# Kernel optimization log

Measured on AMD Instinct MI355X. Metric: run time of the kernel, lower is better.

## Reference

```python
import jax, jax.numpy as jnp
import numpy as np

N = 50000      # num nodes
E = 800000     # edges per hypergraph (avg degree 16)
G = 3          # hyper_edge_num
D_IN = 128
D_OUT = 128


def setup_inputs() -> dict:
    key = jax.random.key(0)
    ks = jax.random.split(key, 6)
    company_emb = jax.random.normal(ks[0], (N, D_IN), dtype=jnp.float32)
    # nn.Linear weight [out, in], glorot-ish scaling
    W = jax.random.normal(ks[1], (D_OUT, D_IN), dtype=jnp.float32) / np.sqrt(D_IN).astype(np.float32)
    alpha = jax.random.normal(ks[2], (G, 1), dtype=jnp.float32)
    edge_rows = jax.random.randint(ks[3], (G, E), 0, N, dtype=jnp.int32)
    edge_cols = jax.random.randint(ks[4], (G, E), 0, N, dtype=jnp.int32)
    edge_vals = jax.random.normal(ks[5], (G, E), dtype=jnp.float32)
    return {
        "company_emb": company_emb,
        "W": W,
        "alpha": alpha,
        "edge_rows": edge_rows,
        "edge_cols": edge_cols,
        "edge_vals": edge_vals,
    }


def reference(company_emb, W, alpha, edge_rows, edge_cols, edge_vals):
    # shared dense projection: h = X @ W^T, [N, D_OUT]
    h = company_emb @ W.T

    def spmm(rows, cols, vals):
        # sparse Laplacian (COO) @ h : gather source rows, scale, scatter-add to dest rows
        msg = vals[:, None] * h[cols]                     # [E, D_OUT]
        return jax.ops.segment_sum(msg, rows, num_segments=N)

    aggs = jax.vmap(spmm)(edge_rows, edge_cols, edge_vals)  # [G, N, D_OUT]
    gate = jax.nn.sigmoid(alpha[:, 0])                       # [G]
    # res = sum_g sigmoid(alpha_g) * (L_g @ h)
    return jnp.einsum('g,gnd->nd', gate, aggs)
```

## Files before the change

kernel.cpp:

```cpp
#include <hip/hip_runtime.h>
#include <math.h>

#define NNODES 50000
#define NEDGE  800000
#define NG     3
#define D      128
#define GE     (NG*NEDGE)
#define NBUK   782
#define CH     4096
#define NBLK   ((GE + CH - 1) / CH)
#define OS     (NBUK + 1)
#define CAP2   3456

typedef __attribute__((ext_vector_type(8))) short bf16x8;
typedef __attribute__((ext_vector_type(4))) float f32x4;

__device__ __forceinline__ unsigned short f2bf(float f) {
    unsigned u = __float_as_uint(f);
    return (unsigned short)((u + 0x7fffu + ((u >> 16) & 1u)) >> 16);
}

__global__ void k_wprep(const float* __restrict__ W, uint4* __restrict__ Wf) {
    const int t = threadIdx.x;
    for (int i = t; i < 2048; i += 256) {
        const int nt   = i >> 8;
        const int kc   = (i >> 6) & 3;
        const int lane = i & 63;
        const int n  = nt * 16 + (lane & 15);
        const int k0 = kc * 32 + (lane >> 4) * 8;
        const float* src = W + (size_t)n * 128 + k0;
        unsigned u0 = (unsigned)f2bf(src[0]) | ((unsigned)f2bf(src[1]) << 16);
        unsigned u1 = (unsigned)f2bf(src[2]) | ((unsigned)f2bf(src[3]) << 16);
        unsigned u2 = (unsigned)f2bf(src[4]) | ((unsigned)f2bf(src[5]) << 16);
        unsigned u3 = (unsigned)f2bf(src[6]) | ((unsigned)f2bf(src[7]) << 16);
        Wf[i] = make_uint4(u0, u1, u2, u3);
    }
}

__global__ __launch_bounds__(256) void k_gemm(const float* __restrict__ X,
                                              const uint4* __restrict__ Wf,
                                              unsigned short* __restrict__ hb16) {
    __shared__ uint4 Wl[2048];
    const int t = threadIdx.x;
#pragma unroll
    for (int j = 0; j < 8; ++j) Wl[t + j * 256] = Wf[t + j * 256];
    __syncthreads();

    const int w    = t >> 6;
    const int lane = t & 63;
    const int q    = lane >> 4;
    const int ml   = lane & 15;
    const int m0   = blockIdx.x * 64 + w * 16;

    int xr = m0 + ml; if (xr >= NNODES) xr = NNODES - 1;
    const float* xrow = X + (size_t)xr * 128;

    bf16x8 xf[4];
#pragma unroll
    for (int kc = 0; kc < 4; ++kc) {
        const int k0 = kc * 32 + q * 8;
        float4 a = *(const float4*)(xrow + k0);
        float4 b = *(const float4*)(xrow + k0 + 4);
        bf16x8 v;
        v[0] = (short)f2bf(a.x); v[1] = (short)f2bf(a.y);
        v[2] = (short)f2bf(a.z); v[3] = (short)f2bf(a.w);
        v[4] = (short)f2bf(b.x); v[5] = (short)f2bf(b.y);
        v[6] = (short)f2bf(b.z); v[7] = (short)f2bf(b.w);
        xf[kc] = v;
    }

#pragma unroll
    for (int nt = 0; nt < 8; ++nt) {
        f32x4 acc = {0.f, 0.f, 0.f, 0.f};
#pragma unroll
        for (int kc = 0; kc < 4; ++kc) {
            const bf16x8 wf = *(const bf16x8*)&Wl[(nt * 4 + kc) * 64 + lane];
            acc = __builtin_amdgcn_mfma_f32_16x16x32_bf16(xf[kc], wf, acc, 0, 0, 0);
        }
#pragma unroll
        for (int r = 0; r < 4; ++r) {
            const int row = m0 + q * 4 + r;
            if (row < NNODES)
                hb16[(size_t)row * 128 + nt * 16 + ml] = f2bf(acc[r]);
        }
    }
}

__global__ __launch_bounds__(256) void k_bin(const int* __restrict__ rows,
                                             const int* __restrict__ cols,
                                             const float* __restrict__ vals,
                                             const float* __restrict__ alpha,
                                             uint2* __restrict__ out1,
                                             int* __restrict__ off1) {
    __shared__ uint2 stg[CH];
    __shared__ unsigned short rnk[CH];
    __shared__ int sA[1024];
    const int t   = threadIdx.x;
    const int blk = blockIdx.x;
    const int start = blk * CH;
    const int end   = (start + CH < GE) ? (start + CH) : GE;

    const float g0 = 1.0f / (1.0f + __expf(-alpha[0]));
    const float g1 = 1.0f / (1.0f + __expf(-alpha[1]));
    const float g2 = 1.0f / (1.0f + __expf(-alpha[2]));

#pragma unroll
    for (int j = 0; j < 4; ++j) sA[t + j * 256] = 0;
    __syncthreads();

    for (int idx = start + t, k = t; idx < end; idx += 256, k += 256) {
        const int r = rows[idx];
        const int c = cols[idx];
        const float v = vals[idx];
        const float gv = v * (idx < NEDGE ? g0 : (idx < 2 * NEDGE ? g1 : g2));
        uint2 rec;
        rec.x = ((unsigned)r << 16) | (unsigned)c;
        rec.y = __float_as_uint(gv);
        stg[k] = rec;
        rnk[k] = (unsigned short)atomicAdd(&sA[r >> 6], 1);
    }
    __syncthreads();

    for (int off = 1; off < 1024; off <<= 1) {
        int v[4];
#pragma unroll
        for (int j = 0; j < 4; ++j) {
            const int i = t + j * 256;
            v[j] = sA[i] + ((i >= off) ? sA[i - off] : 0);
        }
        __syncthreads();
#pragma unroll
        for (int j = 0; j < 4; ++j) sA[t + j * 256] = v[j];
        __syncthreads();
    }

    for (int b = t; b < NBUK; b += 256)
        off1[(size_t)blk * OS + b] = b ? sA[b - 1] : 0;
    if (t == 0) off1[(size_t)blk * OS + NBUK] = sA[NBUK - 1];

    for (int idx = start + t, k = t; idx < end; idx += 256, k += 256) {
        const uint2 rec = stg[k];
        const int b = (int)(rec.x >> 22);
        const int pos = (b ? sA[b - 1] : 0) + (int)rnk[k];
        out1[(size_t)blk * CH + pos] = rec;
    }
}

__global__ __launch_bounds__(512) void k_agg2(const unsigned* __restrict__ hbits,
                                              const uint2* __restrict__ out1,
                                              const int* __restrict__ off1,
                                              float* __restrict__ out) {
    __shared__ uint2 stg[CAP2];
    __shared__ unsigned short order[CAP2];
    __shared__ int sA[512];
    __shared__ int sB[512];
    __shared__ int rh[64], rbase[64], rcur[64];
    const int t = threadIdx.x;
    const int b = blockIdx.x;

    if (t < 64) rh[t] = 0;

    const int s0 = off1[(size_t)t * OS + b];
    const int e0 = off1[(size_t)t * OS + b + 1];
    int s1 = 0, e1 = 0;
    int myLen = e0 - s0;
    if (t + 512 < NBLK) {
        s1 = off1[(size_t)(t + 512) * OS + b];
        e1 = off1[(size_t)(t + 512) * OS + b + 1];
        myLen += e1 - s1;
    }
    sA[t] = myLen;
    __syncthreads();

    int* src = sA; int* dst = sB;
    for (int off = 1; off < 512; off <<= 1) {
        dst[t] = src[t] + ((t >= off) ? src[t - off] : 0);
        __syncthreads();
        int* tmp = src; src = dst; dst = tmp;
    }
    const int base = src[t] - myLen;

    {
        int p = base;
        const uint2* seg = out1 + (size_t)t * CH;
        for (int i = s0; i < e0; ++i, ++p) {
            if (p < CAP2) {
                const uint2 rec = seg[i];
                stg[p] = rec;
                atomicAdd(&rh[(rec.x >> 16) & 63u], 1);
            }
        }
        if (t + 512 < NBLK) {
            const uint2* seg2 = out1 + (size_t)(t + 512) * CH;
            for (int i = s1; i < e1; ++i, ++p) {
                if (p < CAP2) {
                    const uint2 rec = seg2[i];
                    stg[p] = rec;
                    atomicAdd(&rh[(rec.x >> 16) & 63u], 1);
                }
            }
        }
    }
    __syncthreads();

    if (t < 64) sA[t] = rh[t];
    __syncthreads();
    for (int off = 1; off < 64; off <<= 1) {
        int v = 0;
        if (t < 64) v = sA[t] + ((t >= off) ? sA[t - off] : 0);
        __syncthreads();
        if (t < 64) sA[t] = v;
        __syncthreads();
    }
    if (t < 64) { rbase[t] = sA[t] - rh[t]; rcur[t] = sA[t] - rh[t]; }
    __syncthreads();

    {
        const int lim = (base + myLen < CAP2) ? (base + myLen) : CAP2;
        for (int k = base; k < lim; ++k) {
            const int lr = (int)((stg[k].x >> 16) & 63u);
            const int pos = atomicAdd(&rcur[lr], 1);
            order[pos] = (unsigned short)k;
        }
    }
    __syncthreads();

    const int w    = t >> 6;
    const int lane = t & 63;
    for (int k = 0; k < 8; ++k) {
        const int lr  = (w << 3) + k;
        const int row = (b << 6) + lr;
        const int s   = rbase[lr];
        const int cnt = rh[lr];
        float2 acc = make_float2(0.f, 0.f);
        int i = 0;
        for (; i + 8 <= cnt; i += 8) {
            int idx8[8];
#pragma unroll
            for (int j = 0; j < 8; ++j) idx8[j] = order[s + i + j];
            uint2 m[8];
#pragma unroll
            for (int j = 0; j < 8; ++j) m[j] = stg[idx8[j]];
            unsigned hb[8];
#pragma unroll
            for (int j = 0; j < 8; ++j)
                hb[j] = hbits[(size_t)(m[j].x & 0xffffu) * 64 + lane];
#pragma unroll
            for (int j = 0; j < 8; ++j) {
                const float v = __uint_as_float(m[j].y);
                acc.x += v * __uint_as_float(hb[j] << 16);
                acc.y += v * __uint_as_float(hb[j] & 0xffff0000u);
            }
        }
        for (; i < cnt; ++i) {
            const uint2 m = stg[order[s + i]];
            const unsigned hbv = hbits[(size_t)(m.x & 0xffffu) * 64 + lane];
            const float v = __uint_as_float(m.y);
            acc.x += v * __uint_as_float(hbv << 16);
            acc.y += v * __uint_as_float(hbv & 0xffff0000u);
        }
        if (row < NNODES)
            ((float2*)out)[(size_t)row * 64 + lane] = acc;
    }
}

extern "C" void kernel_launch(void* const* d_in, const int* in_sizes, int n_in,
                              void* d_out, int out_size, void* d_ws, size_t ws_size,
                              hipStream_t stream) {
    const float* X     = (const float*)d_in[0];
    const float* W     = (const float*)d_in[1];
    const float* alpha = (const float*)d_in[2];
    const int*   rows  = (const int*)d_in[3];
    const int*   cols  = (const int*)d_in[4];
    const float* vals  = (const float*)d_in[5];
    float* out = (float*)d_out;

    char* ws = (char*)d_ws;
    unsigned*       hbits = (unsigned*)(ws + 0);
    unsigned short* hb16  = (unsigned short*)(ws + 0);
    uint2*          out1  = (uint2*)(ws + 12800000);
    int*            off1  = (int*)  (ws + 32002048);
    uint4*          Wf    = (uint4*)(ws + 33837408);

    hipLaunchKernelGGL(k_wprep, dim3(1), dim3(256), 0, stream, W, Wf);
    hipLaunchKernelGGL(k_gemm, dim3(NBUK), dim3(256), 0, stream, X, Wf, hb16);
    hipLaunchKernelGGL(k_bin, dim3(NBLK), dim3(256), 0, stream,
                       rows, cols, vals, alpha, out1, off1);
    hipLaunchKernelGGL(k_agg2, dim3(NBUK), dim3(512), 0, stream,
                       hbits, out1, off1, out);
}
```

Before: 240.1 us.

## Rebucket rows into 768 variable-width buckets and sort edges directly into SoA shared layout

Destination rows are binned into 768 buckets of about 65 rows each (computed as r*48/3125), so the aggregation grid matches a multiple of the CU count. The aggregation kernel drops the per-thread prefix scan and indirect order array. It counts rows in a first pass, then scatters column indices and values straight into padded structure-of-arrays shared buffers. This allows vectorised 16-byte LDS reads of eight edges at a time, at the cost of reading each segment from global memory twice and clamping buckets that exceed the 4096-entry capacity.

```diff
diff --git a/kernel.cpp b/kernel.cpp
--- a/kernel.cpp
+++ b/kernel.cpp
@@ -6,11 +6,12 @@
 #define NG     3
 #define D      128
 #define GE     (NG*NEDGE)
-#define NBUK   782
+#define NBUK   768
+#define GEMMB  782
 #define CH     4096
 #define NBLK   ((GE + CH - 1) / CH)
 #define OS     (NBUK + 1)
-#define CAP2   3456
+#define CAP    4096
 
 typedef __attribute__((ext_vector_type(8))) short bf16x8;
 typedef __attribute__((ext_vector_type(4))) float f32x4;
@@ -18,6 +19,10 @@
 __device__ __forceinline__ unsigned short f2bf(float f) {
     unsigned u = __float_as_uint(f);
     return (unsigned short)((u + 0x7fffu + ((u >> 16) & 1u)) >> 16);
+}
+
+__device__ __forceinline__ int bucket_of(unsigned r) {
+    return (int)((r * 48u) / 3125u);
 }
 
 __global__ void k_wprep(const float* __restrict__ W, uint4* __restrict__ Wf) {
@@ -117,7 +122,7 @@
         rec.x = ((unsigned)r << 16) | (unsigned)c;
         rec.y = __float_as_uint(gv);
         stg[k] = rec;
-        rnk[k] = (unsigned short)atomicAdd(&sA[r >> 6], 1);
+        rnk[k] = (unsigned short)atomicAdd(&sA[bucket_of((unsigned)r)], 1);
     }
     __syncthreads();
 
@@ -140,127 +145,125 @@
 
     for (int idx = start + t, k = t; idx < end; idx += 256, k += 256) {
         const uint2 rec = stg[k];
-        const int b = (int)(rec.x >> 22);
+        const int b = bucket_of(rec.x >> 16);
         const int pos = (b ? sA[b - 1] : 0) + (int)rnk[k];
         out1[(size_t)blk * CH + pos] = rec;
     }
 }
 
-__global__ __launch_bounds__(512) void k_agg2(const unsigned* __restrict__ hbits,
+__global__ __launch_bounds__(512) void k_agg3(const unsigned* __restrict__ hbits,
                                               const uint2* __restrict__ out1,
                                               const int* __restrict__ off1,
                                               float* __restrict__ out) {
-    __shared__ uint2 stg[CAP2];
-    __shared__ unsigned short order[CAP2];
-    __shared__ int sA[512];
-    __shared__ int sB[512];
-    __shared__ int rh[64], rbase[64], rcur[64];
+    __shared__ __align__(16) unsigned short colS[CAP];
+    __shared__ __align__(16) float          valS[CAP];
+    __shared__ int rh[72], rbase[72], rcur[72];
+    __shared__ int sS[128];
     const int t = threadIdx.x;
     const int b = blockIdx.x;
 
-    if (t < 64) rh[t] = 0;
+    const int sstart = (b * 3125 + 47) / 48;
+    const int send   = ((b + 1) * 3125 + 47) / 48;
+    const int width  = send - sstart;
+
+    if (t < 72) rh[t] = 0;
 
     const int s0 = off1[(size_t)t * OS + b];
     const int e0 = off1[(size_t)t * OS + b + 1];
     int s1 = 0, e1 = 0;
-    int myLen = e0 - s0;
     if (t + 512 < NBLK) {
         s1 = off1[(size_t)(t + 512) * OS + b];
         e1 = off1[(size_t)(t + 512) * OS + b + 1];
-        myLen += e1 - s1;
-    }
-    sA[t] = myLen;
-    __syncthreads();
-
-    int* src = sA; int* dst = sB;
-    for (int off = 1; off < 512; off <<= 1) {
-        dst[t] = src[t] + ((t >= off) ? src[t - off] : 0);
-        __syncthreads();
-        int* tmp = src; src = dst; dst = tmp;
-    }
-    const int base = src[t] - myLen;
+    }
+    __syncthreads();
 
     {
-        int p = base;
         const uint2* seg = out1 + (size_t)t * CH;
-        for (int i = s0; i < e0; ++i, ++p) {
-            if (p < CAP2) {
-                const uint2 rec = seg[i];
-                stg[p] = rec;
-                atomicAdd(&rh[(rec.x >> 16) & 63u], 1);
+        for (int i = s0; i < e0; ++i)
+            atomicAdd(&rh[(int)(seg[i].x >> 16) - sstart], 1);
+        const uint2* seg2 = out1 + (size_t)(t + 512) * CH;
+        for (int i = s1; i < e1; ++i)
+            atomicAdd(&rh[(int)(seg2[i].x >> 16) - sstart], 1);
+    }
+    __syncthreads();
+
+    if (t < 128) sS[t] = (t < width) ? ((rh[t] + 7) & ~7) : 0;
+    __syncthreads();
+    for (int off = 1; off < 128; off <<= 1) {
+        int v = 0;
+        if (t < 128) v = sS[t] + ((t >= off) ? sS[t - off] : 0);
+        __syncthreads();
+        if (t < 128) sS[t] = v;
+        __syncthreads();
+    }
+    if (t < width) {
+        const int rb = sS[t] - ((rh[t] + 7) & ~7);
+        rbase[t] = rb;
+        rcur[t]  = rb;
+    }
+    __syncthreads();
+
+    {
+        const uint2* seg = out1 + (size_t)t * CH;
+        for (int i = s0; i < e0; ++i) {
+            const uint2 rec = seg[i];
+            const int lr  = (int)(rec.x >> 16) - sstart;
+            const int pos = atomicAdd(&rcur[lr], 1);
+            if (pos < CAP) {
+                colS[pos] = (unsigned short)(rec.x & 0xffffu);
+                valS[pos] = __uint_as_float(rec.y);
             }
         }
-        if (t + 512 < NBLK) {
-            const uint2* seg2 = out1 + (size_t)(t + 512) * CH;
-            for (int i = s1; i < e1; ++i, ++p) {
-                if (p < CAP2) {
-                    const uint2 rec = seg2[i];
-                    stg[p] = rec;
-                    atomicAdd(&rh[(rec.x >> 16) & 63u], 1);
-                }
+        const uint2* seg2 = out1 + (size_t)(t + 512) * CH;
+        for (int i = s1; i < e1; ++i) {
+            const uint2 rec = seg2[i];
+            const int lr  = (int)(rec.x >> 16) - sstart;
+            const int pos = atomicAdd(&rcur[lr], 1);
+            if (pos < CAP) {
+                colS[pos] = (unsigned short)(rec.x & 0xffffu);
+                valS[pos] = __uint_as_float(rec.y);
             }
-        }
-    }
-    __syncthreads();
-
-    if (t < 64) sA[t] = rh[t];
-    __syncthreads();
-    for (int off = 1; off < 64; off <<= 1) {
-        int v = 0;
-        if (t < 64) v = sA[t] + ((t >= off) ? sA[t - off] : 0);
-        __syncthreads();
-        if (t < 64) sA[t] = v;
-        __syncthreads();
-    }
-    if (t < 64) { rbase[t] = sA[t] - rh[t]; rcur[t] = sA[t] - rh[t]; }
-    __syncthreads();
-
-    {
-        const int lim = (base + myLen < CAP2) ? (base + myLen) : CAP2;
-        for (int k = base; k < lim; ++k) {
-            const int lr = (int)((stg[k].x >> 16) & 63u);
-            const int pos = atomicAdd(&rcur[lr], 1);
-            order[pos] = (unsigned short)k;
         }
     }
     __syncthreads();
 
     const int w    = t >> 6;
     const int lane = t & 63;
-    for (int k = 0; k < 8; ++k) {
-        const int lr  = (w << 3) + k;
-        const int row = (b << 6) + lr;
-        const int s   = rbase[lr];
-        const int cnt = rh[lr];
+    for (int lr = w; lr < width; lr += 8) {
+        const int s = rbase[lr];
+        int cnt = rh[lr];
+        if (s + cnt > CAP) cnt = (CAP > s) ? (CAP - s) : 0;
         float2 acc = make_float2(0.f, 0.f);
         int i = 0;
         for (; i + 8 <= cnt; i += 8) {
-            int idx8[8];
-#pragma unroll
-            for (int j = 0; j < 8; ++j) idx8[j] = order[s + i + j];
-            uint2 m[8];
-#pragma unroll
-            for (int j = 0; j < 8; ++j) m[j] = stg[idx8[j]];
+            const uint4  cv = *(const uint4*)&colS[s + i];
+            const float4 va = *(const float4*)&valS[s + i];
+            const float4 vb = *(const float4*)&valS[s + i + 4];
             unsigned hb[8];
-#pragma unroll
-            for (int j = 0; j < 8; ++j)
-                hb[j] = hbits[(size_t)(m[j].x & 0xffffu) * 64 + lane];
+            hb[0] = hbits[(size_t)(cv.x & 0xffffu) * 64 + lane];
+            hb[1] = hbits[(size_t)(cv.x >> 16)     * 64 + lane];
+            hb[2] = hbits[(size_t)(cv.y & 0xffffu) * 64 + lane];
+            hb[3] = hbits[(size_t)(cv.y >> 16)     * 64 + lane];
+            hb[4] = hbits[(size_t)(cv.z & 0xffffu) * 64 + lane];
+            hb[5] = hbits[(size_t)(cv.z >> 16)     * 64 + lane];
+            hb[6] = hbits[(size_t)(cv.w & 0xffffu) * 64 + lane];
+            hb[7] = hbits[(size_t)(cv.w >> 16)     * 64 + lane];
+            const float vv[8] = {va.x, va.y, va.z, va.w, vb.x, vb.y, vb.z, vb.w};
 #pragma unroll
             for (int j = 0; j < 8; ++j) {
-                const float v = __uint_as_float(m[j].y);
-                acc.x += v * __uint_as_float(hb[j] << 16);
-                acc.y += v * __uint_as_float(hb[j] & 0xffff0000u);
+                acc.x += vv[j] * __uint_as_float(hb[j] << 16);
+                acc.y += vv[j] * __uint_as_float(hb[j] & 0xffff0000u);
             }
         }
         for (; i < cnt; ++i) {
-            const uint2 m = stg[order[s + i]];
-            const unsigned hbv = hbits[(size_t)(m.x & 0xffffu) * 64 + lane];
-            const float v = __uint_as_float(m.y);
+            const unsigned c   = colS[s + i];
+            const float    v   = valS[s + i];
+            const unsigned hbv = hbits[(size_t)c * 64 + lane];
             acc.x += v * __uint_as_float(hbv << 16);
             acc.y += v * __uint_as_float(hbv & 0xffff0000u);
         }
-        if (row < NNODES)
-            ((float2*)out)[(size_t)row * 64 + lane] = acc;
+        const int row = sstart + lr;
+        ((float2*)out)[(size_t)row * 64 + lane] = acc;
     }
 }
 
@@ -283,9 +286,9 @@
     uint4*          Wf    = (uint4*)(ws + 33837408);
 
     hipLaunchKernelGGL(k_wprep, dim3(1), dim3(256), 0, stream, W, Wf);
-    hipLaunchKernelGGL(k_gemm, dim3(NBUK), dim3(256), 0, stream, X, Wf, hb16);
+    hipLaunchKernelGGL(k_gemm, dim3(GEMMB), dim3(256), 0, stream, X, Wf, hb16);
     hipLaunchKernelGGL(k_bin, dim3(NBLK), dim3(256), 0, stream,
                        rows, cols, vals, alpha, out1, off1);
-    hipLaunchKernelGGL(k_agg2, dim3(NBUK), dim3(512), 0, stream,
+    hipLaunchKernelGGL(k_agg3, dim3(NBUK), dim3(512), 0, stream,
                        hbits, out1, off1, out);
 }
```

After: 257.2 us. 7.2% more time.
